# Kernel optimization log

Hardware: AMD Instinct MI355X
Metric: run time of the kernel (lower is better)

The kernel has to match this reference:

```python
import jax, jax.numpy as jnp
import numpy as np

NUM_BINS = 3
TAIL_BOUND = 1.0


def conv3x3(x, w, b):
    # x: [B,C,H,W], w: [O,I,3,3]
    y = jax.lax.conv_general_dilated(x, w, (1, 1), 'SAME',
                                     dimension_numbers=('NCHW', 'OIHW', 'NCHW'))
    return y + b[None, :, None, None]


def unconstrained_linear_spline(inputs, unnormalized_pdf, tail_bound=TAIL_BOUND):
    # inputs: [B,C,H,W]; unnormalized_pdf: [B,C,H,W,num_bins]
    num_bins = unnormalized_pdf.shape[-1]
    left = bottom = -tail_bound
    right = top = tail_bound
    inside = (inputs >= left) & (inputs <= right)

    x = (inputs - left) / (right - left)  # scale to [0,1]
    pdf = jax.nn.softmax(unnormalized_pdf, axis=-1)
    cdf = jnp.cumsum(pdf, axis=-1)
    cdf = cdf.at[..., -1].set(1.0)
    cdf = jnp.pad(cdf, [(0, 0)] * (cdf.ndim - 1) + [(1, 0)])  # [..., num_bins+1]

    pos = jnp.clip(x, 0.0, 1.0) * num_bins  # clip keeps bin idx valid for outside elems
    bin_idx = jnp.clip(jnp.floor(pos).astype(jnp.int32), 0, num_bins - 1)
    alpha = pos - bin_idx.astype(pos.dtype)

    input_pdfs = jnp.take_along_axis(pdf, bin_idx[..., None], axis=-1)[..., 0]
    out = jnp.take_along_axis(cdf, bin_idx[..., None], axis=-1)[..., 0] + alpha * input_pdfs
    out = jnp.clip(out, 0.0, 1.0)
    lad = jnp.log(input_pdfs) + jnp.log(jnp.asarray(num_bins, pos.dtype))

    out = out * (top - bottom) + bottom
    lad = lad - jnp.log(jnp.asarray(top - bottom, pos.dtype)) + jnp.log(jnp.asarray(right - left, pos.dtype))

    out = jnp.where(inside, out, inputs)       # identity tails
    lad = jnp.where(inside, lad, 0.0)
    return out, lad


def setup_inputs() -> dict:
    key = jax.random.key(0)
    ks = jax.random.split(key, 4)
    B, C, H, W = 32, 64, 64, 64
    hidden = 128
    c_half = C // 2
    c_out = c_half * NUM_BINS
    x = jax.random.normal(ks[0], (B, C, H, W), dtype=jnp.float32)
    objective = jnp.zeros((B,), dtype=jnp.float32)
    W1 = jax.random.normal(ks[1], (hidden, c_half, 3, 3), dtype=jnp.float32) * 0.05
    b1 = jnp.zeros((hidden,), dtype=jnp.float32)
    W2 = jax.random.normal(ks[2], (c_out, hidden, 3, 3), dtype=jnp.float32) * 0.05
    b2 = jnp.zeros((c_out,), dtype=jnp.float32)
    return {'x': x, 'objective': objective, 'W1': W1, 'b1': b1, 'W2': W2, 'b2': b2}


def reference(x, objective, W1, b1, W2, b2):
    identity_split, transform_split = jnp.split(x, 2, axis=1)
    h = jax.nn.relu(conv3x3(identity_split, W1, b1))
    transform_params = conv3x3(h, W2, b2)  # [B, C/2*num_bins, H, W]
    b, c, hh, ww = transform_split.shape
    transform_params = transform_params.reshape(b, c, NUM_BINS, hh, ww).transpose(0, 1, 3, 4, 2)
    transformed, logabsdet = unconstrained_linear_spline(transform_split, transform_params)
    output = jnp.concatenate([identity_split, transformed], axis=1)
    objective_out = objective + jnp.sum(logabsdet.reshape(b, -1), axis=1)
    return output, objective_out
```

## Files before the change

### kernel.cpp

```cpp
#include <hip/hip_runtime.h>

typedef __attribute__((ext_vector_type(8))) __bf16 bf16x8;
typedef __attribute__((ext_vector_type(4))) float f32x4;

__device__ __forceinline__ unsigned short f2bf(float f) {
    unsigned int u = __builtin_bit_cast(unsigned int, f);
    u = (u + 0x7FFFu + ((u >> 16) & 1u)) >> 16;
    return (unsigned short)u;
}

__global__ void __launch_bounds__(256) prep_w(const float* __restrict__ W1,
                                              const float* __restrict__ W2,
                                              unsigned short* __restrict__ Wt1,
                                              unsigned short* __restrict__ Wt2) {
    int tid = blockIdx.x * 256 + threadIdx.x;
    if (tid < 36864) {
        int tt = tid % 9, rem = tid / 9;
        int i = rem & 31, o = rem >> 5;
        Wt1[(tt * 128 + o) * 32 + i] = f2bf(W1[tid]);
    }
    if (tid < 110592) {
        int tt = tid % 9, rem = tid / 9;
        int i = rem & 127, o = rem >> 7;
        int kc = i >> 6, ii = i & 63;
        Wt2[(((kc * 9 + tt) * 96 + o) * 64) + ii] = f2bf(W2[tid]);
    }
}

__global__ void __launch_bounds__(256) conv1_fused(const float* __restrict__ x,
                                                   const float* __restrict__ obj,
                                                   const float* __restrict__ b1,
                                                   const unsigned short* __restrict__ Wt1,
                                                   unsigned short* __restrict__ hbuf,
                                                   float* __restrict__ out) {
    const int LW = 40;
    __shared__ unsigned short sx[6 * 66 * LW];
    int wg = blockIdx.x;
    int b = wg >> 4, h0 = (wg & 15) << 2;
    int t = threadIdx.x;

#pragma unroll
    for (int j = 0; j < 8; ++j) {
        int idx = j * 256 + t;
        int c = idx >> 6, row = (idx >> 4) & 3, w4 = idx & 15;
        size_t off = (((size_t)b * 64 + c) * 64 + (h0 + row)) * 16 + w4;
        reinterpret_cast<float4*>(out)[off] =
            reinterpret_cast<const float4*>(x)[off];
    }
    if (wg == 0 && t < 32) out[8388608 + t] = obj[t];

    if (t < 48) {
        int row = t >> 3, k = t & 7;
        int col = (k & 1) ? 65 : 0, c0 = (k >> 1) * 8;
        *reinterpret_cast<uint4*>(&sx[(row * 66 + col) * LW + c0]) = uint4{0, 0, 0, 0};
    }
    {
        int w = t & 63, c4 = t >> 6;
        const float* xb = x + (size_t)b * 262144;
#pragma unroll
        for (int row = 0; row < 6; ++row) {
            int gh = h0 - 1 + row;
            if (gh >= 0 && gh < 64) {
                const float* xr = xb + (size_t)gh * 64;
#pragma unroll
                for (int co = 0; co < 8; ++co) {
                    int c = co * 4 + c4;
                    sx[(row * 66 + w + 1) * LW + c] = f2bf(xr[(size_t)c * 4096 + w]);
                }
            } else {
#pragma unroll
                for (int co = 0; co < 8; ++co) {
                    int c = co * 4 + c4;
                    sx[(row * 66 + w + 1) * LW + c] = 0;
                }
            }
        }
    }
    __syncthreads();

    int wid = t >> 6, lane = t & 63;
    int lrow = lane & 15, kgrp = lane >> 4;

    bf16x8 afr[2][9];
#pragma unroll
    for (int m2 = 0; m2 < 2; ++m2) {
        int o = (wid * 2 + m2) * 16 + lrow;
#pragma unroll
        for (int tap = 0; tap < 9; ++tap)
            afr[m2][tap] = *reinterpret_cast<const bf16x8*>(
                Wt1 + (size_t)(tap * 128 + o) * 32 + kgrp * 8);
    }

    for (int nt = 0; nt < 16; ++nt) {
        int r = nt >> 2, ww = ((nt & 3) << 4) + lrow;
        f32x4 acc0 = {0.f, 0.f, 0.f, 0.f}, acc1 = {0.f, 0.f, 0.f, 0.f};
#pragma unroll
        for (int dh = 0; dh < 3; ++dh)
#pragma unroll
            for (int dw = 0; dw < 3; ++dw) {
                int tap = dh * 3 + dw;
                bf16x8 bfr = *reinterpret_cast<const bf16x8*>(
                    &sx[((r + dh) * 66 + ww + dw) * LW + kgrp * 8]);
                acc0 = __builtin_amdgcn_mfma_f32_16x16x32_bf16(afr[0][tap], bfr, acc0, 0, 0, 0);
                acc1 = __builtin_amdgcn_mfma_f32_16x16x32_bf16(afr[1][tap], bfr, acc1, 0, 0, 0);
            }
        int hh = h0 + r;
        size_t obase = (((size_t)b * 64 + hh) * 64 + ww) * 128;
#pragma unroll
        for (int m2 = 0; m2 < 2; ++m2) {
            f32x4 a = (m2 == 0) ? acc0 : acc1;
            int o0 = (wid * 2 + m2) * 16 + kgrp * 4;
            unsigned short r4[4];
#pragma unroll
            for (int j = 0; j < 4; ++j) {
                float v = a[j] + b1[o0 + j];
                r4[j] = f2bf(fmaxf(v, 0.f));
            }
            uint2 pk;
            pk.x = (unsigned)r4[0] | ((unsigned)r4[1] << 16);
            pk.y = (unsigned)r4[2] | ((unsigned)r4[3] << 16);
            *reinterpret_cast<uint2*>(hbuf + obase + o0) = pk;
        }
    }
}

__global__ void __launch_bounds__(512) conv2_spline(const unsigned short* __restrict__ hbuf,
                                                    const float* __restrict__ b2,
                                                    const unsigned short* __restrict__ Wt2,
                                                    const float* __restrict__ x,
                                                    float* __restrict__ out) {
    const int LWA = 72;
    const int LWW = 72;
    __shared__ unsigned short sa[6 * 66 * LWA];
    __shared__ unsigned short sw[96 * LWW];
    __shared__ float red[8];
    float* pm = reinterpret_cast<float*>(sa);

    int raw = blockIdx.x;
    int wg = (raw & 7) * 64 + (raw >> 3);
    int b = wg >> 4, h0 = (wg & 15) << 2;
    int t = threadIdx.x;
    int wid = t >> 6, lane = t & 63;
    int lrow = lane & 15, kgrp = lane >> 4;
    int mgrp = wid >> 2, ngrp = wid & 3;
    int mb = mgrp * 3;

    int wo_a = t >> 3, wk_a = t & 7;
    int wdst_a = wo_a * LWW + wk_a * 8;
    int wsrc_a = wo_a * 64 + wk_a * 8;
    int f2 = 512 + t;
    int wo_b = f2 >> 3, wk_b = f2 & 7;
    int wdst_b = wo_b * LWW + wk_b * 8;
    int wsrc_b = wo_b * 64 + wk_b * 8;

    f32x4 acc[3][4];
#pragma unroll
    for (int i = 0; i < 3; ++i)
#pragma unroll
        for (int j = 0; j < 4; ++j) acc[i][j] = f32x4{0.f, 0.f, 0.f, 0.f};

    {
        uint4 v1 = *reinterpret_cast<const uint4*>(Wt2 + wsrc_a);
        *reinterpret_cast<uint4*>(&sw[wdst_a]) = v1;
        if (t < 256) {
            uint4 v2 = *reinterpret_cast<const uint4*>(Wt2 + wsrc_b);
            *reinterpret_cast<uint4*>(&sw[wdst_b]) = v2;
        }
    }

    for (int kc2 = 0; kc2 < 2; ++kc2) {
#pragma unroll
        for (int j = 0; j < 6; ++j) {
            int idx = j * 512 + t;
            int row = idx >> 9, rem = idx & 511;
            int w = rem >> 3, c0 = (rem & 7) * 8;
            int gh = h0 - 1 + row;
            uint4 v = uint4{0, 0, 0, 0};
            if (gh >= 0 && gh < 64)
                v = *reinterpret_cast<const uint4*>(
                    hbuf + (((size_t)b * 64 + gh) * 64 + w) * 128 + kc2 * 64 + c0);
            *reinterpret_cast<uint4*>(&sa[(row * 66 + (w + 1)) * LWA + c0]) = v;
        }
        if (t < 96) {
            int row = t >> 4, k = t & 15;
            int col = (k & 1) ? 65 : 0, c0 = (k >> 1) * 8;
            *reinterpret_cast<uint4*>(&sa[(row * 66 + col) * LWA + c0]) = uint4{0, 0, 0, 0};
        }
        __syncthreads();

        for (int tap = 0; tap < 9; ++tap) {
            int s = kc2 * 9 + tap;
            uint4 v1, v2;
            if (s < 17) {
                const unsigned short* wsrc = Wt2 + (size_t)(s + 1) * 6144;
                v1 = *reinterpret_cast<const uint4*>(wsrc + wsrc_a);
                if (t < 256) v2 = *reinterpret_cast<const uint4*>(wsrc + wsrc_b);
            }

            int dh = tap / 3, dw = tap % 3;
            bf16x8 wfr[3][2];
#pragma unroll
            for (int mi = 0; mi < 3; ++mi) {
                int o = (mb + mi) * 16 + lrow;
                wfr[mi][0] = *reinterpret_cast<const bf16x8*>(&sw[o * LWW + kgrp * 8]);
                wfr[mi][1] = *reinterpret_cast<const bf16x8*>(&sw[o * LWW + 32 + kgrp * 8]);
            }
#pragma unroll
            for (int ni = 0; ni < 4; ++ni) {
                int nt = ngrp * 4 + ni;
                int rr = nt >> 2, wcol = (nt & 3) * 16 + lrow;
                int base = ((rr + dh) * 66 + wcol + dw) * LWA;
                bf16x8 a0 = *reinterpret_cast<const bf16x8*>(&sa[base + kgrp * 8]);
                bf16x8 a1 = *reinterpret_cast<const bf16x8*>(&sa[base + 32 + kgrp * 8]);
#pragma unroll
                for (int mi = 0; mi < 3; ++mi) {
                    acc[mi][ni] = __builtin_amdgcn_mfma_f32_16x16x32_bf16(wfr[mi][0], a0, acc[mi][ni], 0, 0, 0);
                    acc[mi][ni] = __builtin_amdgcn_mfma_f32_16x16x32_bf16(wfr[mi][1], a1, acc[mi][ni], 0, 0, 0);
                }
            }
            __syncthreads();
            if (s < 17) {
                *reinterpret_cast<uint4*>(&sw[wdst_a]) = v1;
                if (t < 256) *reinterpret_cast<uint4*>(&sw[wdst_b]) = v2;
            }
            __syncthreads();
        }
    }

    float lad_acc = 0.f;
    for (int half = 0; half < 2; ++half) {
        __syncthreads();
        if ((ngrp >> 1) == half) {
#pragma unroll
            for (int mi = 0; mi < 3; ++mi) {
                int o0 = (mb + mi) * 16 + kgrp * 4;
                float bb0 = b2[o0], bb1 = b2[o0 + 1], bb2 = b2[o0 + 2], bb3 = b2[o0 + 3];
#pragma unroll
                for (int ni = 0; ni < 4; ++ni) {
                    int p = (ngrp & 1) * 64 + ni * 16 + lrow;
                    f32x4 v = acc[mi][ni];
                    pm[p * 101 + o0]     = v[0] + bb0;
                    pm[p * 101 + o0 + 1] = v[1] + bb1;
                    pm[p * 101 + o0 + 2] = v[2] + bb2;
                    pm[p * 101 + o0 + 3] = v[3] + bb3;
                }
            }
        }
        __syncthreads();
#pragma unroll 4
        for (int it = 0; it < 8; ++it) {
            int idx = it * 512 + t;
            int c = idx >> 7, p = idx & 127;
            int pos = half * 128 + p;
            int pb = p * 101 + 3 * c;
            float u0 = pm[pb];
            float u1 = pm[pb + 1];
            float u2 = pm[pb + 2];
            size_t gpos = (size_t)(b * 64 + 32 + c) * 4096 + (size_t)(h0 + (pos >> 6)) * 64 + (pos & 63);
            float xin = x[gpos];
            float mx = fmaxf(u0, fmaxf(u1, u2));
            float e0 = __expf(u0 - mx), e1 = __expf(u1 - mx), e2 = __expf(u2 - mx);
            float s = e0 + e1 + e2;
            float inv = 1.0f / s;
            float pos01 = fminf(fmaxf((xin + 1.f) * 0.5f, 0.f), 1.f) * 3.f;
            int bin = (int)pos01; bin = bin > 2 ? 2 : bin;
            float alpha = pos01 - (float)bin;
            float eb = (bin == 0) ? e0 : ((bin == 1) ? e1 : e2);
            float cb = (bin == 0) ? 0.f : ((bin == 1) ? e0 : (e0 + e1));
            float pk = eb * inv;
            float outv = cb * inv + alpha * pk;
            outv = fminf(fmaxf(outv, 0.f), 1.f) * 2.f - 1.f;
            float lad = __logf(pk) + 1.09861228866810969f;
            bool inside = (xin >= -1.f) && (xin <= 1.f);
            if (!inside) { outv = xin; lad = 0.f; }
            out[gpos] = outv;
            lad_acc += lad;
        }
    }
#pragma unroll
    for (int off = 32; off > 0; off >>= 1)
        lad_acc += __shfl_down(lad_acc, off, 64);
    if (lane == 0) red[wid] = lad_acc;
    __syncthreads();
    if (t == 0) {
        float s = 0.f;
#pragma unroll
        for (int i = 0; i < 8; ++i) s += red[i];
        atomicAdd(out + 8388608 + b, s);
    }
}

extern "C" void kernel_launch(void* const* d_in, const int* in_sizes, int n_in,
                              void* d_out, int out_size, void* d_ws, size_t ws_size,
                              hipStream_t stream) {
    const float* x   = (const float*)d_in[0];
    const float* obj = (const float*)d_in[1];
    const float* W1  = (const float*)d_in[2];
    const float* b1  = (const float*)d_in[3];
    const float* W2  = (const float*)d_in[4];
    const float* b2  = (const float*)d_in[5];
    float* out = (float*)d_out;
    char* ws = (char*)d_ws;

    unsigned short* hbuf = (unsigned short*)ws;
    unsigned short* Wt1  = (unsigned short*)(ws + 33554432);
    unsigned short* Wt2  = (unsigned short*)(ws + 33554432 + 73728);

    hipLaunchKernelGGL(prep_w,       dim3(432), dim3(256), 0, stream, W1, W2, Wt1, Wt2);
    hipLaunchKernelGGL(conv1_fused,  dim3(512), dim3(256), 0, stream, x, obj, b1, Wt1, hbuf, out);
    hipLaunchKernelGGL(conv2_spline, dim3(512), dim3(512), 0, stream, hbuf, b2, Wt2, x, out);
}
```

Baseline: 73.85 us.

## Double-buffer conv2 weight tiles in LDS with fragment-ordered prepacked layout

Prepacks W2 so each tap's 96x64 bf16 slice is stored in the exact per-lane MFMA fragment order, letting the global-to-LDS copy be a flat contiguous transfer and fragment reads conflict-free. The LDS weight tile is double-buffered, which removes one of the two barriers per tap since the next tap's weights go to the other buffer. LDS use grows by one extra weight tile, which could affect occupancy.

```diff
diff --git a/kernel.cpp b/kernel.cpp
--- a/kernel.cpp
+++ b/kernel.cpp
@@ -23,7 +23,11 @@
         int tt = tid % 9, rem = tid / 9;
         int i = rem & 127, o = rem >> 7;
         int kc = i >> 6, ii = i & 63;
-        Wt2[(((kc * 9 + tt) * 96 + o) * 64) + ii] = f2bf(W2[tid]);
+        int khalf = ii >> 5, kgrp = (ii >> 3) & 3, j = ii & 7;
+        int o_tile = o >> 4, lrow = o & 15;
+        int s = kc * 9 + tt;
+        Wt2[(size_t)s * 6144 +
+            (size_t)(((o_tile * 2 + khalf) * 64 + kgrp * 16 + lrow) * 8 + j)] = f2bf(W2[tid]);
     }
 }
 
@@ -130,9 +134,8 @@
                                                     const float* __restrict__ x,
                                                     float* __restrict__ out) {
     const int LWA = 72;
-    const int LWW = 72;
-    __shared__ unsigned short sa[6 * 66 * LWA];
-    __shared__ unsigned short sw[96 * LWW];
+    __shared__ __align__(16) unsigned short sa[6 * 66 * LWA];
+    __shared__ __align__(16) unsigned short swd[2 * 6144];
     __shared__ float red[8];
     float* pm = reinterpret_cast<float*>(sa);
 
@@ -145,14 +148,6 @@
     int mgrp = wid >> 2, ngrp = wid & 3;
     int mb = mgrp * 3;
 
-    int wo_a = t >> 3, wk_a = t & 7;
-    int wdst_a = wo_a * LWW + wk_a * 8;
-    int wsrc_a = wo_a * 64 + wk_a * 8;
-    int f2 = 512 + t;
-    int wo_b = f2 >> 3, wk_b = f2 & 7;
-    int wdst_b = wo_b * LWW + wk_b * 8;
-    int wsrc_b = wo_b * 64 + wk_b * 8;
-
     f32x4 acc[3][4];
 #pragma unroll
     for (int i = 0; i < 3; ++i)
@@ -160,12 +155,11 @@
         for (int j = 0; j < 4; ++j) acc[i][j] = f32x4{0.f, 0.f, 0.f, 0.f};
 
     {
-        uint4 v1 = *reinterpret_cast<const uint4*>(Wt2 + wsrc_a);
-        *reinterpret_cast<uint4*>(&sw[wdst_a]) = v1;
-        if (t < 256) {
-            uint4 v2 = *reinterpret_cast<const uint4*>(Wt2 + wsrc_b);
-            *reinterpret_cast<uint4*>(&sw[wdst_b]) = v2;
-        }
+        *reinterpret_cast<uint4*>(&swd[t * 8]) =
+            *reinterpret_cast<const uint4*>(Wt2 + t * 8);
+        if (t < 256)
+            *reinterpret_cast<uint4*>(&swd[(512 + t) * 8]) =
+                *reinterpret_cast<const uint4*>(Wt2 + (512 + t) * 8);
     }
 
     for (int kc2 = 0; kc2 < 2; ++kc2) {
@@ -190,20 +184,24 @@
 
         for (int tap = 0; tap < 9; ++tap) {
             int s = kc2 * 9 + tap;
+            unsigned short* swc = swd + (s & 1) * 6144;
+            unsigned short* swn = swd + ((s + 1) & 1) * 6144;
             uint4 v1, v2;
             if (s < 17) {
                 const unsigned short* wsrc = Wt2 + (size_t)(s + 1) * 6144;
-                v1 = *reinterpret_cast<const uint4*>(wsrc + wsrc_a);
-                if (t < 256) v2 = *reinterpret_cast<const uint4*>(wsrc + wsrc_b);
+                v1 = *reinterpret_cast<const uint4*>(wsrc + t * 8);
+                if (t < 256) v2 = *reinterpret_cast<const uint4*>(wsrc + (512 + t) * 8);
             }
 
             int dh = tap / 3, dw = tap % 3;
             bf16x8 wfr[3][2];
 #pragma unroll
             for (int mi = 0; mi < 3; ++mi) {
-                int o = (mb + mi) * 16 + lrow;
-                wfr[mi][0] = *reinterpret_cast<const bf16x8*>(&sw[o * LWW + kgrp * 8]);
-                wfr[mi][1] = *reinterpret_cast<const bf16x8*>(&sw[o * LWW + 32 + kgrp * 8]);
+                int ot = mb + mi;
+                wfr[mi][0] = *reinterpret_cast<const bf16x8*>(
+                    &swc[((ot * 2 + 0) * 64 + lane) * 8]);
+                wfr[mi][1] = *reinterpret_cast<const bf16x8*>(
+                    &swc[((ot * 2 + 1) * 64 + lane) * 8]);
             }
 #pragma unroll
             for (int ni = 0; ni < 4; ++ni) {
@@ -218,10 +216,9 @@
                     acc[mi][ni] = __builtin_amdgcn_mfma_f32_16x16x32_bf16(wfr[mi][1], a1, acc[mi][ni], 0, 0, 0);
                 }
             }
-            __syncthreads();
             if (s < 17) {
-                *reinterpret_cast<uint4*>(&sw[wdst_a]) = v1;
-                if (t < 256) *reinterpret_cast<uint4*>(&sw[wdst_b]) = v2;
+                *reinterpret_cast<uint4*>(&swn[t * 8]) = v1;
+                if (t < 256) *reinterpret_cast<uint4*>(&swn[(512 + t) * 8]) = v2;
             }
             __syncthreads();
         }
```

New measurement: 71.49 us. -3.2%, faster.
